# Optimization experiments

Measured on AMD Instinct MI355X. Metric: run time of the kernel, lower is better.

## Reference

```python
import jax, jax.numpy as jnp
import numpy as np

NUM_PARAMS = 8          # number of generalized coordinates q
DIM = 2 * NUM_PARAMS    # state = (q, q_dot)
HID = 128               # hidden width of the Lagrangian MLP
BATCH = 4096


def _linear_init(key, fan_in, fan_out):
    # torch nn.Linear default init: U(-1/sqrt(fan_in), 1/sqrt(fan_in))
    lim = 1.0 / np.sqrt(fan_in)
    kw, kb = jax.random.split(key)
    W = jax.random.uniform(kw, (fan_out, fan_in), minval=-lim, maxval=lim, dtype=jnp.float32)
    b = jax.random.uniform(kb, (fan_out,), minval=-lim, maxval=lim, dtype=jnp.float32)
    return W, b


def setup_inputs() -> dict:
    key = jax.random.key(0)
    ks = jax.random.split(key, 6)
    W1, b1 = _linear_init(ks[0], DIM, HID)
    W2, b2 = _linear_init(ks[1], HID, HID)
    W3, b3 = _linear_init(ks[2], HID, HID)
    W4, b4 = _linear_init(ks[3], HID, HID)
    W5, b5 = _linear_init(ks[4], HID, 1)
    x = jax.random.normal(ks[5], (BATCH, DIM), dtype=jnp.float32)
    return {"x": x, "W1": W1, "b1": b1, "W2": W2, "b2": b2,
            "W3": W3, "b3": b3, "W4": W4, "b4": b4, "W5": W5, "b5": b5}


def reference(x, W1, b1, W2, b2, W3, b3, W4, b4, W5, b5):
    n = NUM_PARAMS

    def lagrangian(xs):  # xs: (DIM,) -> scalar L
        h = jax.nn.softplus(W1 @ xs + b1)
        h = jax.nn.softplus(W2 @ h + b2)
        h = jax.nn.softplus(W3 @ h + b3)
        h = jax.nn.softplus(W4 @ h + b4)
        return (W5 @ h + b5)[0]

    def per_sample(xs):
        J = jax.grad(lagrangian)(xs)            # (DIM,) = dL/dx
        H = jax.hessian(lagrangian)(xs)         # (DIM, DIM)
        A = J[:n]                               # dL/dq
        B = H[n:, n:]                           # d2L/dq_dot dq_dot
        C = H[n:, :n]                           # d2L/dq_dot dq
        # q_ddot = pinv(B) @ (dL/dq - d2L/dq_dot dq @ q_dot)
        return jnp.linalg.pinv(B) @ (A - C @ xs[n:])

    return jax.vmap(per_sample)(x)              # (BATCH, NUM_PARAMS)
```

## Files before the change

### kernel.cpp

```cpp
#include <hip/hip_runtime.h>
#include <math.h>

#define NPAR 8
#define DIM  16
#define HID  128
#define BATCH 4096
#define VSTRF 132
#define NVEC 9

typedef float v2f __attribute__((ext_vector_type(2)));
typedef float v4f __attribute__((ext_vector_type(4)));

#define PKFMA(d, a, b) asm("v_pk_fma_f32 %0, %1, %2, %0" : "+v"(d) : "v"(a), "v"(b))

__device__ float g_wsf[6*HID*HID + HID*DIM];

__device__ __forceinline__ float sigf(float z){ return 1.0f/(1.0f+__expf(-z)); }
__device__ __forceinline__ float spf(float z){ return fmaxf(z,0.0f)+log1pf(__expf(-fabsf(z))); }

__global__ __launch_bounds__(256)
void pack_weights(const float* __restrict__ W1, const float* __restrict__ W2,
                  const float* __restrict__ W3, const float* __restrict__ W4) {
  int t = blockIdx.x*blockDim.x + threadIdx.x;
  int p4 = t*4;
  float4 r;
  if (p4 < 6*HID*HID) {
    int ri = p4 >> 14;
    const float* W = (ri < 2) ? W2 : ((ri < 4) ? W3 : W4);
    int p  = p4 & 16383;
    int low = p & 127;
    int B  = p >> 7;
    int jo = (B & 3)*32 + (low >> 2);
    int T  = B >> 2;
    int kr0 = (T >> 4)*64 + (T & 15)*4;
    if ((ri & 1) == 0) {
      r = *((const float4*)(W + jo*HID + kr0));
    } else {
      r.x = W[(kr0+0)*HID + jo];
      r.y = W[(kr0+1)*HID + jo];
      r.z = W[(kr0+2)*HID + jo];
      r.w = W[(kr0+3)*HID + jo];
    }
  } else {
    int rr = p4 - 6*HID*HID;
    int k0 = (rr >> 6)*4;
    int m2 = (rr >> 2) & 15;
    r.x = W1[(k0+0)*DIM + m2];
    r.y = W1[(k0+1)*DIM + m2];
    r.z = W1[(k0+2)*DIM + m2];
    r.w = W1[(k0+3)*DIM + m2];
  }
  *((float4*)(g_wsf + p4)) = r;
}

__device__ __forceinline__ void gemv9f32(const float* __restrict__ Wbase,
    const float* __restrict__ bin, int o, int kh, int w, float* z) {
  const v4f* Wq = (const v4f*)Wbase;
  const float* hb = bin + kh*64;
  v2f acc0[NVEC], acc1[NVEC];
#pragma unroll
  for (int v=0;v<NVEC;++v){ acc0[v]=(v2f){0.0f,0.0f}; acc1[v]=(v2f){0.0f,0.0f}; }
#pragma unroll 2
  for (int q=0;q<16;++q){
    int base = ((kh*16+q)*4)*32 + w*64 + o;
    v4f w0 = Wq[base], w1 = Wq[base+32];
    v2f w0a=w0.xy, w0b=w0.zw;
    v2f w1a=w1.xy, w1b=w1.zw;
#pragma unroll
    for (int v=0;v<NVEC;++v){
      v4f h = *((const v4f*)(hb + v*VSTRF + 4*q));
      v2f ha=h.xy, hc=h.zw;
      PKFMA(acc0[v], w0a, ha); PKFMA(acc0[v], w0b, hc);
      PKFMA(acc1[v], w1a, ha); PKFMA(acc1[v], w1b, hc);
    }
  }
#pragma unroll
  for (int v=0;v<NVEC;++v){
    float u0 = acc0[v].x + acc0[v].y;
    float u1 = acc1[v].x + acc1[v].y;
    u0 += __shfl_xor(u0,32);
    u1 += __shfl_xor(u1,32);
    z[v] = kh ? u1 : u0;
  }
}

__global__ __launch_bounds__(128)
__attribute__((amdgpu_waves_per_eu(5)))
void lnn_main(const float* __restrict__ x, const float* __restrict__ W1,
              const float* __restrict__ b1, const float* __restrict__ b2,
              const float* __restrict__ b3, const float* __restrict__ b4,
              const float* __restrict__ W5, float* __restrict__ out) {
  const int t  = threadIdx.x;
  const int l  = t & 63;
  const int o  = l & 31;
  const int kh = l >> 5;
  const int w  = t >> 6;
  const int j  = w*64 + 32*kh + o;
  const int s  = blockIdx.x;

  __shared__ __align__(16) float buf[NVEC*VSTRF];
  __shared__ float xs[16];
  __shared__ float hH[8*16];
  __shared__ float hJs[16];

  if (t < DIM) xs[t] = x[s*DIM + t];
  __syncthreads();

  const float4* W1v = (const float4*)W1;
  float s1;
  float w1f[8];
  {
    float4 a0 = W1v[j*4+0], a1 = W1v[j*4+1], a2 = W1v[j*4+2], a3 = W1v[j*4+3];
    float z1 = b1[j];
    z1 = fmaf(a0.x, xs[0],  z1); z1 = fmaf(a0.y, xs[1],  z1);
    z1 = fmaf(a0.z, xs[2],  z1); z1 = fmaf(a0.w, xs[3],  z1);
    z1 = fmaf(a1.x, xs[4],  z1); z1 = fmaf(a1.y, xs[5],  z1);
    z1 = fmaf(a1.z, xs[6],  z1); z1 = fmaf(a1.w, xs[7],  z1);
    z1 = fmaf(a2.x, xs[8],  z1); z1 = fmaf(a2.y, xs[9],  z1);
    z1 = fmaf(a2.z, xs[10], z1); z1 = fmaf(a2.w, xs[11], z1);
    z1 = fmaf(a3.x, xs[12], z1); z1 = fmaf(a3.y, xs[13], z1);
    z1 = fmaf(a3.z, xs[14], z1); z1 = fmaf(a3.w, xs[15], z1);
    s1 = sigf(z1);
    buf[j] = spf(z1);
    w1f[0]=a2.x; w1f[1]=a2.y; w1f[2]=a2.z; w1f[3]=a2.w;
    w1f[4]=a3.x; w1f[5]=a3.y; w1f[6]=a3.z; w1f[7]=a3.w;
#pragma unroll
    for (int i=0;i<8;++i) buf[(1+i)*VSTRF + j] = s1*w1f[i];
  }
  __syncthreads();

  float z[NVEC];

  gemv9f32(g_wsf + 0, buf, o, kh, w, z);
  float z2 = z[0] + b2[j];
  float t2[8];
#pragma unroll
  for (int i=0;i<8;++i) t2[i] = z[1+i];
  float s2 = sigf(z2);
  __syncthreads();
  buf[j] = spf(z2);
#pragma unroll
  for (int i=0;i<8;++i) buf[(1+i)*VSTRF + j] = s2*z[1+i];
  __syncthreads();

  gemv9f32(g_wsf + 32768, buf, o, kh, w, z);
  float z3 = z[0] + b3[j];
  float t3[8];
#pragma unroll
  for (int i=0;i<8;++i) t3[i] = z[1+i];
  float s3 = sigf(z3);
  __syncthreads();
  buf[j] = spf(z3);
#pragma unroll
  for (int i=0;i<8;++i) buf[(1+i)*VSTRF + j] = s3*z[1+i];
  __syncthreads();

  gemv9f32(g_wsf + 65536, buf, o, kh, w, z);
  {
    float z4 = z[0] + b4[j];
    float w5 = W5[j];
    float sa = sigf(z4);
    float ca = w5*sa*(1.0f-sa);
    __syncthreads();
    buf[j] = w5*sa;
#pragma unroll
    for (int i=0;i<8;++i) buf[(1+i)*VSTRF + j] = ca*z[1+i];
  }
  __syncthreads();

  gemv9f32(g_wsf + 81920, buf, o, kh, w, z);
  {
    float da = s3*(1.0f-s3)*z[0];
    __syncthreads();
    buf[j] = z[0]*s3;
#pragma unroll
    for (int i=0;i<8;++i) buf[(1+i)*VSTRF + j] = fmaf(z[1+i], s3, da*t3[i]);
  }
  __syncthreads();

  gemv9f32(g_wsf + 49152, buf, o, kh, w, z);
  {
    float da = s2*(1.0f-s2)*z[0];
    __syncthreads();
    buf[j] = z[0]*s2;
#pragma unroll
    for (int i=0;i<8;++i) buf[(1+i)*VSTRF + j] = fmaf(z[1+i], s2, da*t2[i]);
  }
  __syncthreads();

  gemv9f32(g_wsf + 16384, buf, o, kh, w, z);
  {
    float da = s1*(1.0f-s1)*z[0];
    __syncthreads();
    buf[j] = z[0]*s1;
#pragma unroll
    for (int i=0;i<8;++i) buf[(1+i)*VSTRF + j] = fmaf(z[1+i], s1, da*w1f[i]);
  }
  __syncthreads();

  {
    const int m = t & 15, dd = t >> 4;
    const v4f* P1 = (const v4f*)(g_wsf + 98304);
    v2f aH={0.0f,0.0f}, aJ={0.0f,0.0f};
#pragma unroll 4
    for (int q=0; q<32; ++q){
      v4f wq = P1[q*DIM + m];
      v2f wa=wq.xy, wb=wq.zw;
      v4f u0 = *((const v4f*)(buf + (1+dd)*VSTRF + 4*q));
      v4f gg = *((const v4f*)(buf + 4*q));
      PKFMA(aH, wa, u0.xy); PKFMA(aH, wb, u0.zw);
      PKFMA(aJ, wa, gg.xy); PKFMA(aJ, wb, gg.zw);
    }
    hH[dd*16 + m] = aH.x + aH.y;
    if (dd == 0) hJs[m] = aJ.x + aJ.y;
  }
  __syncthreads();

  if (t < 64) {
    const int r = t >> 3, c = t & 7;
    float Bv = hH[r*16 + 8 + c];
    float Cr = hH[r*16 + c];
    float Jr = hJs[r];
    float p0 = Cr * xs[8 + c];
    p0 += __shfl_xor(p0, 1); p0 += __shfl_xor(p0, 2); p0 += __shfl_xor(p0, 4);
    float rhs = Jr - p0;

    float Bt = __shfl(Bv, c*8 + r);
    float Am = 0.5f*(Bv + Bt);
    float Vm = (r == c) ? 1.0f : 0.0f;

    for (int sweep = 0; sweep < 4; ++sweep) {
#pragma unroll
      for (int rr = 0; rr < 7; ++rr) {
        int pc = (c == 7) ? rr : ((c == rr) ? 7 : (2*rr + 7 - c) % 7);
        int cp = min(c, pc), cq = max(c, pc);
        float App = __shfl(Am, cp*8+cp);
        float Aqq = __shfl(Am, cq*8+cq);
        float Apq = __shfl(Am, cp*8+cq);
        float tau = (Aqq - App) / (2.0f*Apq);
        float tt  = (tau >= 0.0f ? 1.0f : -1.0f) / (fabsf(tau) + sqrtf(1.0f + tau*tau));
        float cth = 1.0f / sqrtf(1.0f + tt*tt);
        float sth = tt * cth;
        if (fabsf(Apq) < 1e-30f) { cth = 1.0f; sth = 0.0f; }
        float cthr = __shfl(cth, r*8+r);
        float sthr = __shfl(sth, r*8+r);
        float Arp = __shfl(Am, r*8+cp);
        float Arq = __shfl(Am, r*8+cq);
        float colv = (c == cp) ? (cth*Arp - sth*Arq) : (sth*Arp + cth*Arq);
        int pr2 = (r == 7) ? rr : ((r == rr) ? 7 : (2*rr + 7 - r) % 7);
        int rp = min(r, pr2), rq = max(r, pr2);
        float Mpc = __shfl(colv, rp*8+c);
        float Mqc = __shfl(colv, rq*8+c);
        Am = (r == rp) ? (cthr*Mpc - sthr*Mqc) : (sthr*Mpc + cthr*Mqc);
        float Vrp = __shfl(Vm, r*8+cp);
        float Vrq = __shfl(Vm, r*8+cq);
        Vm = (c == cp) ? (cth*Vrp - sth*Vrq) : (sth*Vrp + cth*Vrq);
      }
    }

    float lam_c = __shfl(Am, c*8 + c);
    float adiag = (r == c) ? fabsf(Am) : 0.0f;
#pragma unroll
    for (int off = 32; off; off >>= 1) adiag = fmaxf(adiag, __shfl_xor(adiag, off));
    float cutoff = 9.5367431640625e-06f * adiag;

    float pr = Vm * rhs;
    pr += __shfl_xor(pr, 8); pr += __shfl_xor(pr, 16); pr += __shfl_xor(pr, 32);
    float ww = (fabsf(lam_c) > cutoff) ? (pr / lam_c) : 0.0f;
    float yr = Vm * ww;
    yr += __shfl_xor(yr, 1); yr += __shfl_xor(yr, 2); yr += __shfl_xor(yr, 4);
    if (c == 0) out[s*NPAR + r] = yr;
  }
}

extern "C" void kernel_launch(void* const* d_in, const int* in_sizes, int n_in,
                              void* d_out, int out_size, void* d_ws, size_t ws_size,
                              hipStream_t stream) {
  (void)in_sizes; (void)n_in; (void)out_size; (void)d_ws; (void)ws_size;
  const float* x  = (const float*)d_in[0];
  const float* W1 = (const float*)d_in[1];
  const float* b1 = (const float*)d_in[2];
  const float* W2 = (const float*)d_in[3];
  const float* b2 = (const float*)d_in[4];
  const float* W3 = (const float*)d_in[5];
  const float* b3 = (const float*)d_in[6];
  const float* W4 = (const float*)d_in[7];
  const float* b4 = (const float*)d_in[8];
  const float* W5 = (const float*)d_in[9];
  float* out = (float*)d_out;

  pack_weights<<<98, 256, 0, stream>>>(W1, W2, W3, W4);
  lnn_main<<<BATCH, 128, 0, stream>>>(x, W1, b1, b2, b3, b4, W5, out);
}
```

Measured before the change: 227.1 us.

## Process two samples per block to reuse weight loads across both

Each block now handles two batch samples, sharing every weight fetch in the GEMV passes between two sets of activation buffers, and the grid is halved. Both waves now run the final eigen-solve in parallel, one sample each. This roughly halves global/L2 weight traffic per sample but doubles accumulator registers, and the waves_per_eu hint is dropped, so occupancy may fall or registers may spill.

```diff
diff --git a/kernel.cpp b/kernel.cpp
--- a/kernel.cpp
+++ b/kernel.cpp
@@ -53,13 +53,18 @@
   *((float4*)(g_wsf + p4)) = r;
 }
 
-__device__ __forceinline__ void gemv9f32(const float* __restrict__ Wbase,
-    const float* __restrict__ bin, int o, int kh, int w, float* z) {
+__device__ __forceinline__ void gemv2(const float* __restrict__ Wbase,
+    const float* __restrict__ bA, const float* __restrict__ bB,
+    int o, int kh, int w, float* zA, float* zB) {
   const v4f* Wq = (const v4f*)Wbase;
-  const float* hb = bin + kh*64;
-  v2f acc0[NVEC], acc1[NVEC];
-#pragma unroll
-  for (int v=0;v<NVEC;++v){ acc0[v]=(v2f){0.0f,0.0f}; acc1[v]=(v2f){0.0f,0.0f}; }
+  const float* hbA = bA + kh*64;
+  const float* hbB = bB + kh*64;
+  v2f a0A[NVEC], a1A[NVEC], a0B[NVEC], a1B[NVEC];
+#pragma unroll
+  for (int v=0;v<NVEC;++v){
+    a0A[v]=(v2f){0.0f,0.0f}; a1A[v]=(v2f){0.0f,0.0f};
+    a0B[v]=(v2f){0.0f,0.0f}; a1B[v]=(v2f){0.0f,0.0f};
+  }
 #pragma unroll 2
   for (int q=0;q<16;++q){
     int base = ((kh*16+q)*4)*32 + w*64 + o;
@@ -68,24 +73,32 @@
     v2f w1a=w1.xy, w1b=w1.zw;
 #pragma unroll
     for (int v=0;v<NVEC;++v){
-      v4f h = *((const v4f*)(hb + v*VSTRF + 4*q));
-      v2f ha=h.xy, hc=h.zw;
-      PKFMA(acc0[v], w0a, ha); PKFMA(acc0[v], w0b, hc);
-      PKFMA(acc1[v], w1a, ha); PKFMA(acc1[v], w1b, hc);
+      v4f hA = *((const v4f*)(hbA + v*VSTRF + 4*q));
+      v4f hB = *((const v4f*)(hbB + v*VSTRF + 4*q));
+      v2f hAa=hA.xy, hAc=hA.zw;
+      v2f hBa=hB.xy, hBc=hB.zw;
+      PKFMA(a0A[v], w0a, hAa); PKFMA(a0A[v], w0b, hAc);
+      PKFMA(a1A[v], w1a, hAa); PKFMA(a1A[v], w1b, hAc);
+      PKFMA(a0B[v], w0a, hBa); PKFMA(a0B[v], w0b, hBc);
+      PKFMA(a1B[v], w1a, hBa); PKFMA(a1B[v], w1b, hBc);
     }
   }
 #pragma unroll
   for (int v=0;v<NVEC;++v){
-    float u0 = acc0[v].x + acc0[v].y;
-    float u1 = acc1[v].x + acc1[v].y;
+    float u0 = a0A[v].x + a0A[v].y;
+    float u1 = a1A[v].x + a1A[v].y;
     u0 += __shfl_xor(u0,32);
     u1 += __shfl_xor(u1,32);
-    z[v] = kh ? u1 : u0;
+    zA[v] = kh ? u1 : u0;
+    float p0 = a0B[v].x + a0B[v].y;
+    float p1 = a1B[v].x + a1B[v].y;
+    p0 += __shfl_xor(p0,32);
+    p1 += __shfl_xor(p1,32);
+    zB[v] = kh ? p1 : p0;
   }
 }
 
 __global__ __launch_bounds__(128)
-__attribute__((amdgpu_waves_per_eu(5)))
 void lnn_main(const float* __restrict__ x, const float* __restrict__ W1,
               const float* __restrict__ b1, const float* __restrict__ b2,
               const float* __restrict__ b3, const float* __restrict__ b4,
@@ -96,132 +109,177 @@
   const int kh = l >> 5;
   const int w  = t >> 6;
   const int j  = w*64 + 32*kh + o;
-  const int s  = blockIdx.x;
-
-  __shared__ __align__(16) float buf[NVEC*VSTRF];
-  __shared__ float xs[16];
-  __shared__ float hH[8*16];
-  __shared__ float hJs[16];
-
-  if (t < DIM) xs[t] = x[s*DIM + t];
+  const int sA = blockIdx.x*2;
+  const int sB = sA + 1;
+
+  __shared__ __align__(16) float bufA[NVEC*VSTRF];
+  __shared__ __align__(16) float bufB[NVEC*VSTRF];
+  __shared__ float xsA[16], xsB[16];
+  __shared__ float hHA[8*16], hHB[8*16];
+  __shared__ float hJA[16], hJB[16];
+
+  if (t < DIM) xsA[t] = x[sA*DIM + t];
+  else if (t >= 64 && t < 64+DIM) xsB[t-64] = x[sB*DIM + (t-64)];
   __syncthreads();
 
   const float4* W1v = (const float4*)W1;
-  float s1;
+  float s1A, s1B;
   float w1f[8];
   {
     float4 a0 = W1v[j*4+0], a1 = W1v[j*4+1], a2 = W1v[j*4+2], a3 = W1v[j*4+3];
-    float z1 = b1[j];
-    z1 = fmaf(a0.x, xs[0],  z1); z1 = fmaf(a0.y, xs[1],  z1);
-    z1 = fmaf(a0.z, xs[2],  z1); z1 = fmaf(a0.w, xs[3],  z1);
-    z1 = fmaf(a1.x, xs[4],  z1); z1 = fmaf(a1.y, xs[5],  z1);
-    z1 = fmaf(a1.z, xs[6],  z1); z1 = fmaf(a1.w, xs[7],  z1);
-    z1 = fmaf(a2.x, xs[8],  z1); z1 = fmaf(a2.y, xs[9],  z1);
-    z1 = fmaf(a2.z, xs[10], z1); z1 = fmaf(a2.w, xs[11], z1);
-    z1 = fmaf(a3.x, xs[12], z1); z1 = fmaf(a3.y, xs[13], z1);
-    z1 = fmaf(a3.z, xs[14], z1); z1 = fmaf(a3.w, xs[15], z1);
-    s1 = sigf(z1);
-    buf[j] = spf(z1);
+    float bj = b1[j];
+    float z1A = bj, z1B = bj;
+    z1A = fmaf(a0.x, xsA[0],  z1A); z1A = fmaf(a0.y, xsA[1],  z1A);
+    z1A = fmaf(a0.z, xsA[2],  z1A); z1A = fmaf(a0.w, xsA[3],  z1A);
+    z1A = fmaf(a1.x, xsA[4],  z1A); z1A = fmaf(a1.y, xsA[5],  z1A);
+    z1A = fmaf(a1.z, xsA[6],  z1A); z1A = fmaf(a1.w, xsA[7],  z1A);
+    z1A = fmaf(a2.x, xsA[8],  z1A); z1A = fmaf(a2.y, xsA[9],  z1A);
+    z1A = fmaf(a2.z, xsA[10], z1A); z1A = fmaf(a2.w, xsA[11], z1A);
+    z1A = fmaf(a3.x, xsA[12], z1A); z1A = fmaf(a3.y, xsA[13], z1A);
+    z1A = fmaf(a3.z, xsA[14], z1A); z1A = fmaf(a3.w, xsA[15], z1A);
+    z1B = fmaf(a0.x, xsB[0],  z1B); z1B = fmaf(a0.y, xsB[1],  z1B);
+    z1B = fmaf(a0.z, xsB[2],  z1B); z1B = fmaf(a0.w, xsB[3],  z1B);
+    z1B = fmaf(a1.x, xsB[4],  z1B); z1B = fmaf(a1.y, xsB[5],  z1B);
+    z1B = fmaf(a1.z, xsB[6],  z1B); z1B = fmaf(a1.w, xsB[7],  z1B);
+    z1B = fmaf(a2.x, xsB[8],  z1B); z1B = fmaf(a2.y, xsB[9],  z1B);
+    z1B = fmaf(a2.z, xsB[10], z1B); z1B = fmaf(a2.w, xsB[11], z1B);
+    z1B = fmaf(a3.x, xsB[12], z1B); z1B = fmaf(a3.y, xsB[13], z1B);
+    z1B = fmaf(a3.z, xsB[14], z1B); z1B = fmaf(a3.w, xsB[15], z1B);
+    s1A = sigf(z1A); s1B = sigf(z1B);
+    bufA[j] = spf(z1A); bufB[j] = spf(z1B);
     w1f[0]=a2.x; w1f[1]=a2.y; w1f[2]=a2.z; w1f[3]=a2.w;
     w1f[4]=a3.x; w1f[5]=a3.y; w1f[6]=a3.z; w1f[7]=a3.w;
 #pragma unroll
-    for (int i=0;i<8;++i) buf[(1+i)*VSTRF + j] = s1*w1f[i];
-  }
-  __syncthreads();
-
-  float z[NVEC];
-
-  gemv9f32(g_wsf + 0, buf, o, kh, w, z);
-  float z2 = z[0] + b2[j];
-  float t2[8];
-#pragma unroll
-  for (int i=0;i<8;++i) t2[i] = z[1+i];
-  float s2 = sigf(z2);
-  __syncthreads();
-  buf[j] = spf(z2);
-#pragma unroll
-  for (int i=0;i<8;++i) buf[(1+i)*VSTRF + j] = s2*z[1+i];
-  __syncthreads();
-
-  gemv9f32(g_wsf + 32768, buf, o, kh, w, z);
-  float z3 = z[0] + b3[j];
-  float t3[8];
-#pragma unroll
-  for (int i=0;i<8;++i) t3[i] = z[1+i];
-  float s3 = sigf(z3);
-  __syncthreads();
-  buf[j] = spf(z3);
-#pragma unroll
-  for (int i=0;i<8;++i) buf[(1+i)*VSTRF + j] = s3*z[1+i];
-  __syncthreads();
-
-  gemv9f32(g_wsf + 65536, buf, o, kh, w, z);
-  {
-    float z4 = z[0] + b4[j];
+    for (int i=0;i<8;++i){
+      bufA[(1+i)*VSTRF + j] = s1A*w1f[i];
+      bufB[(1+i)*VSTRF + j] = s1B*w1f[i];
+    }
+  }
+  __syncthreads();
+
+  float zA[NVEC], zB[NVEC];
+
+  gemv2(g_wsf + 0, bufA, bufB, o, kh, w, zA, zB);
+  float z2A = zA[0] + b2[j], z2B = zB[0] + b2[j];
+  float t2A[8], t2B[8];
+#pragma unroll
+  for (int i=0;i<8;++i){ t2A[i] = zA[1+i]; t2B[i] = zB[1+i]; }
+  float s2A = sigf(z2A), s2B = sigf(z2B);
+  __syncthreads();
+  bufA[j] = spf(z2A); bufB[j] = spf(z2B);
+#pragma unroll
+  for (int i=0;i<8;++i){
+    bufA[(1+i)*VSTRF + j] = s2A*zA[1+i];
+    bufB[(1+i)*VSTRF + j] = s2B*zB[1+i];
+  }
+  __syncthreads();
+
+  gemv2(g_wsf + 32768, bufA, bufB, o, kh, w, zA, zB);
+  float z3A = zA[0] + b3[j], z3B = zB[0] + b3[j];
+  float t3A[8], t3B[8];
+#pragma unroll
+  for (int i=0;i<8;++i){ t3A[i] = zA[1+i]; t3B[i] = zB[1+i]; }
+  float s3A = sigf(z3A), s3B = sigf(z3B);
+  __syncthreads();
+  bufA[j] = spf(z3A); bufB[j] = spf(z3B);
+#pragma unroll
+  for (int i=0;i<8;++i){
+    bufA[(1+i)*VSTRF + j] = s3A*zA[1+i];
+    bufB[(1+i)*VSTRF + j] = s3B*zB[1+i];
+  }
+  __syncthreads();
+
+  gemv2(g_wsf + 65536, bufA, bufB, o, kh, w, zA, zB);
+  {
+    float z4A = zA[0] + b4[j], z4B = zB[0] + b4[j];
     float w5 = W5[j];
-    float sa = sigf(z4);
-    float ca = w5*sa*(1.0f-sa);
+    float saA = sigf(z4A), saB = sigf(z4B);
+    float caA = w5*saA*(1.0f-saA), caB = w5*saB*(1.0f-saB);
     __syncthreads();
-    buf[j] = w5*sa;
-#pragma unroll
-    for (int i=0;i<8;++i) buf[(1+i)*VSTRF + j] = ca*z[1+i];
-  }
-  __syncthreads();
-
-  gemv9f32(g_wsf + 81920, buf, o, kh, w, z);
-  {
-    float da = s3*(1.0f-s3)*z[0];
+    bufA[j] = w5*saA; bufB[j] = w5*saB;
+#pragma unroll
+    for (int i=0;i<8;++i){
+      bufA[(1+i)*VSTRF + j] = caA*zA[1+i];
+      bufB[(1+i)*VSTRF + j] = caB*zB[1+i];
+    }
+  }
+  __syncthreads();
+
+  gemv2(g_wsf + 81920, bufA, bufB, o, kh, w, zA, zB);
+  {
+    float daA = s3A*(1.0f-s3A)*zA[0], daB = s3B*(1.0f-s3B)*zB[0];
     __syncthreads();
-    buf[j] = z[0]*s3;
-#pragma unroll
-    for (int i=0;i<8;++i) buf[(1+i)*VSTRF + j] = fmaf(z[1+i], s3, da*t3[i]);
-  }
-  __syncthreads();
-
-  gemv9f32(g_wsf + 49152, buf, o, kh, w, z);
-  {
-    float da = s2*(1.0f-s2)*z[0];
+    bufA[j] = zA[0]*s3A; bufB[j] = zB[0]*s3B;
+#pragma unroll
+    for (int i=0;i<8;++i){
+      bufA[(1+i)*VSTRF + j] = fmaf(zA[1+i], s3A, daA*t3A[i]);
+      bufB[(1+i)*VSTRF + j] = fmaf(zB[1+i], s3B, daB*t3B[i]);
+    }
+  }
+  __syncthreads();
+
+  gemv2(g_wsf + 49152, bufA, bufB, o, kh, w, zA, zB);
+  {
+    float daA = s2A*(1.0f-s2A)*zA[0], daB = s2B*(1.0f-s2B)*zB[0];
     __syncthreads();
-    buf[j] = z[0]*s2;
-#pragma unroll
-    for (int i=0;i<8;++i) buf[(1+i)*VSTRF + j] = fmaf(z[1+i], s2, da*t2[i]);
-  }
-  __syncthreads();
-
-  gemv9f32(g_wsf + 16384, buf, o, kh, w, z);
-  {
-    float da = s1*(1.0f-s1)*z[0];
+    bufA[j] = zA[0]*s2A; bufB[j] = zB[0]*s2B;
+#pragma unroll
+    for (int i=0;i<8;++i){
+      bufA[(1+i)*VSTRF + j] = fmaf(zA[1+i], s2A, daA*t2A[i]);
+      bufB[(1+i)*VSTRF + j] = fmaf(zB[1+i], s2B, daB*t2B[i]);
+    }
+  }
+  __syncthreads();
+
+  gemv2(g_wsf + 16384, bufA, bufB, o, kh, w, zA, zB);
+  {
+    float daA = s1A*(1.0f-s1A)*zA[0], daB = s1B*(1.0f-s1B)*zB[0];
     __syncthreads();
-    buf[j] = z[0]*s1;
-#pragma unroll
-    for (int i=0;i<8;++i) buf[(1+i)*VSTRF + j] = fmaf(z[1+i], s1, da*w1f[i]);
+    bufA[j] = zA[0]*s1A; bufB[j] = zB[0]*s1B;
+#pragma unroll
+    for (int i=0;i<8;++i){
+      bufA[(1+i)*VSTRF + j] = fmaf(zA[1+i], s1A, daA*w1f[i]);
+      bufB[(1+i)*VSTRF + j] = fmaf(zB[1+i], s1B, daB*w1f[i]);
+    }
   }
   __syncthreads();
 
   {
     const int m = t & 15, dd = t >> 4;
     const v4f* P1 = (const v4f*)(g_wsf + 98304);
-    v2f aH={0.0f,0.0f}, aJ={0.0f,0.0f};
+    v2f aHA={0.0f,0.0f}, aJA={0.0f,0.0f};
+    v2f aHB={0.0f,0.0f}, aJB={0.0f,0.0f};
 #pragma unroll 4
     for (int q=0; q<32; ++q){
       v4f wq = P1[q*DIM + m];
       v2f wa=wq.xy, wb=wq.zw;
-      v4f u0 = *((const v4f*)(buf + (1+dd)*VSTRF + 4*q));
-      v4f gg = *((const v4f*)(buf + 4*q));
-      PKFMA(aH, wa, u0.xy); PKFMA(aH, wb, u0.zw);
-      PKFMA(aJ, wa, gg.xy); PKFMA(aJ, wb, gg.zw);
-    }
-    hH[dd*16 + m] = aH.x + aH.y;
-    if (dd == 0) hJs[m] = aJ.x + aJ.y;
-  }
-  __syncthreads();
-
-  if (t < 64) {
-    const int r = t >> 3, c = t & 7;
+      v4f u0A = *((const v4f*)(bufA + (1+dd)*VSTRF + 4*q));
+      v4f ggA = *((const v4f*)(bufA + 4*q));
+      v4f u0B = *((const v4f*)(bufB + (1+dd)*VSTRF + 4*q));
+      v4f ggB = *((const v4f*)(bufB + 4*q));
+      v2f uAa=u0A.xy, uAc=u0A.zw, gAa=ggA.xy, gAc=ggA.zw;
+      v2f uBa=u0B.xy, uBc=u0B.zw, gBa=ggB.xy, gBc=ggB.zw;
+      PKFMA(aHA, wa, uAa); PKFMA(aHA, wb, uAc);
+      PKFMA(aJA, wa, gAa); PKFMA(aJA, wb, gAc);
+      PKFMA(aHB, wa, uBa); PKFMA(aHB, wb, uBc);
+      PKFMA(aJB, wa, gBa); PKFMA(aJB, wb, gBc);
+    }
+    hHA[dd*16 + m] = aHA.x + aHA.y;
+    hHB[dd*16 + m] = aHB.x + aHB.y;
+    if (dd == 0) { hJA[m] = aJA.x + aJA.y; hJB[m] = aJB.x + aJB.y; }
+  }
+  __syncthreads();
+
+  {
+    const int r = l >> 3, c = l & 7;
+    const float* hH  = w ? hHB : hHA;
+    const float* hJs = w ? hJB : hJA;
+    const float* xsP = w ? xsB : xsA;
+    const int so = w ? sB : sA;
     float Bv = hH[r*16 + 8 + c];
     float Cr = hH[r*16 + c];
     float Jr = hJs[r];
-    float p0 = Cr * xs[8 + c];
+    float p0 = Cr * xsP[8 + c];
     p0 += __shfl_xor(p0, 1); p0 += __shfl_xor(p0, 2); p0 += __shfl_xor(p0, 4);
     float rhs = Jr - p0;
 
@@ -269,7 +327,7 @@
     float ww = (fabsf(lam_c) > cutoff) ? (pr / lam_c) : 0.0f;
     float yr = Vm * ww;
     yr += __shfl_xor(yr, 1); yr += __shfl_xor(yr, 2); yr += __shfl_xor(yr, 4);
-    if (c == 0) out[s*NPAR + r] = yr;
+    if (c == 0) out[so*NPAR + r] = yr;
   }
 }
 
@@ -290,5 +348,5 @@
   float* out = (float*)d_out;
 
   pack_weights<<<98, 256, 0, stream>>>(W1, W2, W3, W4);
-  lnn_main<<<BATCH, 128, 0, stream>>>(x, W1, b1, b2, b3, b4, W5, out);
+  lnn_main<<<BATCH/2, 128, 0, stream>>>(x, W1, b1, b2, b3, b4, W5, out);
 }
```

Result: no change. 230.9 us (+1.7%).
